# Kernel tuning notes

Hardware: AMD Instinct MI355X
Metric: run time of the kernel (lower is better)

The kernel has to match this reference:

```python
import jax, jax.numpy as jnp
import numpy as np

ROUTING = 3
N_VERTEX = 32
D_CAP = 16
MULT_D = 64
B = 64
T_DIMS = {"text": 128, "audio": 512, "video": 256, "frames": 256}


def _xavier(key, shape):
    # torch xavier_normal_ on (T, n, MULT_d, d_c): receptive = MULT_d*d_c
    T, n, j, d = shape
    recep = j * d
    std = np.sqrt(2.0 / (n * recep + T * recep))
    return jax.random.normal(key, shape, dtype=jnp.float32) * std


def setup_inputs() -> dict:
    key = jax.random.key(0)
    ks = jax.random.split(key, 8)
    inp = {}
    for i, (name, T) in enumerate(T_DIMS.items()):
        inp[name] = jax.random.normal(ks[i], (B, T, MULT_D), dtype=jnp.float32)
    wnames = ["W_tpc", "W_apc", "W_vpc", "W_fpc"]
    for i, (name, (_, T)) in enumerate(zip(wnames, T_DIMS.items())):
        inp[name] = _xavier(ks[4 + i], (T, N_VERTEX, MULT_D, D_CAP))
    return inp


def _route(pri, routing):
    # pri: [B, T, n, d_c]; routing uses detached (stop-gradient) capsules
    pri_sg = jax.lax.stop_gradient(pri)
    Bn, T, n, d = pri.shape
    b = jnp.zeros((Bn, T, n), dtype=pri.dtype)
    for _ in range(routing):
        rc = jax.nn.softmax(b, axis=2)                      # [B, T, n]
        v = jnp.tanh(jnp.einsum('btnd,btn->bnd', pri_sg, rc))
        b = b + jnp.einsum('bnd,btnd->btn', v, pri_sg)      # agreement update
    rc = jnp.softmax(b, axis=2) if False else jax.nn.softmax(b, axis=2)
    # final vertex uses non-detached capsules with last routing coefficients
    return jnp.tanh(jnp.einsum('btnd,btn->bnd', pri, rc))


def reference(text, audio, video, frames, W_tpc, W_apc, W_vpc, W_fpc):
    outs = []
    for x, W in ((text, W_tpc), (audio, W_apc), (video, W_vpc), (frames, W_fpc)):
        pri = jnp.einsum('btj,tnjd->btnd', x, W)  # primary capsules [B,T,n,d_c]
        outs.append(_route(pri, ROUTING))
    return tuple(outs)
```

## Files before the change

kernel.cpp:

```cpp
#include <hip/hip_runtime.h>


typedef __attribute__((ext_vector_type(8))) short short8;
typedef __attribute__((ext_vector_type(4))) float floatx4;

#define PRI_BYTES 75497472ull

static __device__ __forceinline__ unsigned short f2bf(float f) {
  union { float f; unsigned int i; } v;
  v.f = f;
  unsigned int x = v.i;
  return (unsigned short)((x + 0x7fffu + ((x >> 16) & 1u)) >> 16);
}

__global__ __launch_bounds__(256) void pri_kernel(
    const float* __restrict__ x0, const float* __restrict__ x1,
    const float* __restrict__ x2, const float* __restrict__ x3,
    const float* __restrict__ w0, const float* __restrict__ w1,
    const float* __restrict__ w2, const float* __restrict__ w3,
    unsigned short* __restrict__ priAll) {
  __shared__ unsigned short wb[256 * 72];
  __shared__ unsigned short sc[4][16][136];

  int blk = blockIdx.x;
  int tid = threadIdx.x;

  int tpair = blk >> 1, half = blk & 1;
  const float* x;
  const float* W;
  unsigned short* priT;
  int T, t;
  if (tpair < 128)      { x = x0; W = w0; priT = priAll;               T = 128; t = tpair; }
  else if (tpair < 640) { x = x1; W = w1; priT = priAll + 4194304ull;  T = 512; t = tpair - 128; }
  else if (tpair < 896) { x = x2; W = w2; priT = priAll + 20971520ull; T = 256; t = tpair - 640; }
  else                  { x = x3; W = w3; priT = priAll + 29360128ull; T = 256; t = tpair - 896; }
  priT += (size_t)t * 32768;

  {
    const floatx4* Wf4 = (const floatx4*)(W + (size_t)t * 32768);
    unsigned int* wb32 = (unsigned int*)wb;
#pragma unroll
    for (int it = 0; it < 8; ++it) {
      int idx = it * 256 + tid;
      int nl = idx >> 7, jp = (idx >> 2) & 31, dq = idx & 3;
      int ng = half * 16 + nl;
      floatx4 fa = Wf4[ng * 256 + (2 * jp) * 4 + dq];
      floatx4 fb = Wf4[ng * 256 + (2 * jp + 1) * 4 + dq];
      int rbase = nl * 16 + dq * 4;
#pragma unroll
      for (int k = 0; k < 4; ++k) {
        unsigned int dw = (unsigned int)f2bf(fa[k]) | ((unsigned int)f2bf(fb[k]) << 16);
        wb32[(rbase + k) * 36 + jp] = dw;
      }
    }
  }

  int lane = tid & 63, mt = tid >> 6;
  int m = lane & 15, q = lane >> 4;
  short8 afrag[2];
  {
    const float* xrow = x + ((size_t)(mt * 16 + m) * T + t) * 64;
#pragma unroll
    for (int s = 0; s < 2; ++s) {
      const floatx4* xp = (const floatx4*)(xrow + s * 32 + q * 8);
      floatx4 u0 = xp[0], u1 = xp[1];
      afrag[s][0] = (short)f2bf(u0[0]); afrag[s][1] = (short)f2bf(u0[1]);
      afrag[s][2] = (short)f2bf(u0[2]); afrag[s][3] = (short)f2bf(u0[3]);
      afrag[s][4] = (short)f2bf(u1[0]); afrag[s][5] = (short)f2bf(u1[1]);
      afrag[s][6] = (short)f2bf(u1[2]); afrag[s][7] = (short)f2bf(u1[3]);
    }
  }
  __syncthreads();

  for (int g = 0; g < 2; ++g) {
#pragma unroll
    for (int k = 0; k < 8; ++k) {
      int nt = g * 8 + k;
      const short8* b0p = (const short8*)&wb[(nt * 16 + m) * 72 + q * 8];
      const short8* b1p = (const short8*)&wb[(nt * 16 + m) * 72 + 32 + q * 8];
      short8 bf0 = *b0p, bf1 = *b1p;
      floatx4 acc = {0.f, 0.f, 0.f, 0.f};
      acc = __builtin_amdgcn_mfma_f32_16x16x32_bf16(afrag[0], bf0, acc, 0, 0, 0);
      acc = __builtin_amdgcn_mfma_f32_16x16x32_bf16(afrag[1], bf1, acc, 0, 0, 0);
#pragma unroll
      for (int reg = 0; reg < 4; ++reg)
        sc[mt][q * 4 + reg][k * 16 + m] = f2bf(acc[reg]);
    }
#pragma unroll
    for (int i = 0; i < 4; ++i) {
      int bl = (lane >> 4) + i * 4;
      int sh = (lane & 15) * 8;
      short8 v = *(const short8*)&sc[mt][bl][sh];
      *(short8*)(priT + (size_t)(mt * 16 + bl) * 512 + half * 256 + g * 128 + sh) = v;
    }
  }
}

__global__ __launch_bounds__(1024) void route_kernel(
    const unsigned short* __restrict__ priAll, float* __restrict__ out) {
  __shared__ float Sl[32][640];
  __shared__ float Vc_s[544];

  int blk = blockIdx.x;
  int mod = blk & 3, b = blk >> 2;
  size_t poff; int T;
  if (mod == 0)      { poff = 0ull;         T = 128; }
  else if (mod == 1) { poff = 4194304ull;   T = 512; }
  else if (mod == 2) { poff = 20971520ull;  T = 256; }
  else               { poff = 29360128ull;  T = 256; }

  const unsigned short* priM = priAll + poff + (size_t)b * 512;

  int tid = threadIdx.x;
  int n = tid & 31, g = tid >> 5;
  int nbase = n * 17;

  if (tid < 544) Vc_s[tid] = 0.f;
  __syncthreads();

  for (int pass = 0; pass < 4; ++pass) {
    float Vc[16];
#pragma unroll
    for (int d = 0; d < 16; ++d) Vc[d] = Vc_s[nbase + d];

    float acc[16];
#pragma unroll
    for (int d = 0; d < 16; ++d) acc[d] = 0.f;

    const unsigned short* pr = priM + (size_t)(g * 2) * 32768 + n * 16;
    uint4 c0a = ((const uint4*)pr)[0], c0b = ((const uint4*)pr)[1];
    uint4 c1a = ((const uint4*)(pr + 32768))[0], c1b = ((const uint4*)(pr + 32768))[1];

    for (int t0 = g * 2; t0 < T; t0 += 64) {
      uint4 n0a, n0b, n1a, n1b;
      if (t0 + 64 < T) {
        const unsigned short* pn = priM + (size_t)(t0 + 64) * 32768 + n * 16;
        n0a = ((const uint4*)pn)[0]; n0b = ((const uint4*)pn)[1];
        n1a = ((const uint4*)(pn + 32768))[0]; n1b = ((const uint4*)(pn + 32768))[1];
      }

#pragma unroll
      for (int tt = 0; tt < 2; ++tt) {
        uint4 ca = tt ? c1a : c0a;
        uint4 cb = tt ? c1b : c0b;
        float p[16];
        {
          unsigned int wds[8] = {ca.x, ca.y, ca.z, ca.w, cb.x, cb.y, cb.z, cb.w};
#pragma unroll
          for (int k = 0; k < 8; ++k) {
            union { unsigned int u; float f; } lo, hi;
            lo.u = wds[k] << 16;
            hi.u = wds[k] & 0xffff0000u;
            p[2 * k] = lo.f;
            p[2 * k + 1] = hi.f;
          }
        }
        float logit = 0.f;
#pragma unroll
        for (int d = 0; d < 16; ++d) logit += p[d] * Vc[d];
        float mx = logit;
#pragma unroll
        for (int o = 16; o >= 1; o >>= 1) mx = fmaxf(mx, __shfl_xor(mx, o, 32));
        float e = __expf(logit - mx);
        float s = e;
#pragma unroll
        for (int o = 16; o >= 1; o >>= 1) s += __shfl_xor(s, o, 32);
        float rc = e / s;
#pragma unroll
        for (int d = 0; d < 16; ++d) acc[d] += rc * p[d];
      }

      if (t0 + 64 < T) { c0a = n0a; c0b = n0b; c1a = n1a; c1b = n1b; }
    }

#pragma unroll
    for (int d = 0; d < 16; ++d) Sl[g][nbase + d] = acc[d];
    __syncthreads();

    if (tid < 512) {
      int nn = tid >> 4, dd = tid & 15;
      int idx = nn * 17 + dd;
      float s = 0.f;
#pragma unroll
      for (int gg = 0; gg < 32; ++gg) s += Sl[gg][idx];
      float v = tanhf(s);
      if (pass == 3) out[(size_t)(mod * 64 + b) * 512 + tid] = v;
      else Vc_s[idx] += v;
    }
    __syncthreads();
  }
}

extern "C" void kernel_launch(void* const* d_in, const int* in_sizes, int n_in,
                              void* d_out, int out_size, void* d_ws, size_t ws_size,
                              hipStream_t stream) {
  const float* x0 = (const float*)d_in[0];
  const float* x1 = (const float*)d_in[1];
  const float* x2 = (const float*)d_in[2];
  const float* x3 = (const float*)d_in[3];
  const float* w0 = (const float*)d_in[4];
  const float* w1 = (const float*)d_in[5];
  const float* w2 = (const float*)d_in[6];
  const float* w3 = (const float*)d_in[7];

  unsigned short* pri = (unsigned short*)d_ws;

  pri_kernel<<<2304, 256, 0, stream>>>(x0, x1, x2, x3, w0, w1, w2, w3, pri);
  route_kernel<<<256, 1024, 0, stream>>>(pri, (float*)d_out);
}
```

Baseline: 262.8 us.

## Process two timesteps per pri block with prefetched weights; simplify routing softmax

Each pri_kernel block now handles two consecutive timesteps, so the grid is halved. The second timestep's weights are loaded into registers while the first is computed, hiding global load latency behind the MFMA work. The route kernel walks one timestep per 32-thread group with a stride of 32 timesteps and drops the max-subtraction in the softmax, removing five shuffles per timestep. Without the max-subtraction the exponentials could overflow if the logits grow large. The extra register arrays per thread may also reduce occupancy.

```diff
diff --git a/kernel.cpp b/kernel.cpp
--- a/kernel.cpp
+++ b/kernel.cpp
@@ -3,8 +3,6 @@
 
 typedef __attribute__((ext_vector_type(8))) short short8;
 typedef __attribute__((ext_vector_type(4))) float floatx4;
-
-#define PRI_BYTES 75497472ull
 
 static __device__ __forceinline__ unsigned short f2bf(float f) {
   union { float f; unsigned int i; } v;
@@ -25,75 +23,130 @@
   int blk = blockIdx.x;
   int tid = threadIdx.x;
 
-  int tpair = blk >> 1, half = blk & 1;
+  int pair = blk >> 1, half = blk & 1;
   const float* x;
   const float* W;
   unsigned short* priT;
-  int T, t;
-  if (tpair < 128)      { x = x0; W = w0; priT = priAll;               T = 128; t = tpair; }
-  else if (tpair < 640) { x = x1; W = w1; priT = priAll + 4194304ull;  T = 512; t = tpair - 128; }
-  else if (tpair < 896) { x = x2; W = w2; priT = priAll + 20971520ull; T = 256; t = tpair - 640; }
-  else                  { x = x3; W = w3; priT = priAll + 29360128ull; T = 256; t = tpair - 896; }
-  priT += (size_t)t * 32768;
-
+  int T, t0;
+  if (pair < 64)       { x = x0; W = w0; priT = priAll;               T = 128; t0 = 2 * pair; }
+  else if (pair < 320) { x = x1; W = w1; priT = priAll + 4194304ull;  T = 512; t0 = 2 * (pair - 64); }
+  else if (pair < 448) { x = x2; W = w2; priT = priAll + 20971520ull; T = 256; t0 = 2 * (pair - 320); }
+  else                 { x = x3; W = w3; priT = priAll + 29360128ull; T = 256; t0 = 2 * (pair - 448); }
+  unsigned short* priT0 = priT + (size_t)t0 * 32768;
+  unsigned short* priT1 = priT + (size_t)(t0 + 1) * 32768;
+
+  int lane = tid & 63, mt = tid >> 6;
+  int m = lane & 15, q = lane >> 4;
+
+  floatx4 xv[8];
   {
-    const floatx4* Wf4 = (const floatx4*)(W + (size_t)t * 32768);
-    unsigned int* wb32 = (unsigned int*)wb;
+    const float* xrow = x + ((size_t)(mt * 16 + m) * T + t0) * 64;
+#pragma unroll
+    for (int tt = 0; tt < 2; ++tt)
+#pragma unroll
+      for (int s = 0; s < 2; ++s) {
+        const floatx4* xp = (const floatx4*)(xrow + tt * 64 + s * 32 + q * 8);
+        xv[tt * 4 + s * 2]     = xp[0];
+        xv[tt * 4 + s * 2 + 1] = xp[1];
+      }
+  }
+
+  floatx4 wra[8], wrb[8];
+  {
+    const floatx4* Wf = (const floatx4*)(W + (size_t)t0 * 32768);
 #pragma unroll
     for (int it = 0; it < 8; ++it) {
       int idx = it * 256 + tid;
       int nl = idx >> 7, jp = (idx >> 2) & 31, dq = idx & 3;
       int ng = half * 16 + nl;
-      floatx4 fa = Wf4[ng * 256 + (2 * jp) * 4 + dq];
-      floatx4 fb = Wf4[ng * 256 + (2 * jp + 1) * 4 + dq];
-      int rbase = nl * 16 + dq * 4;
-#pragma unroll
-      for (int k = 0; k < 4; ++k) {
-        unsigned int dw = (unsigned int)f2bf(fa[k]) | ((unsigned int)f2bf(fb[k]) << 16);
-        wb32[(rbase + k) * 36 + jp] = dw;
-      }
-    }
-  }
-
-  int lane = tid & 63, mt = tid >> 6;
-  int m = lane & 15, q = lane >> 4;
-  short8 afrag[2];
+      wra[it] = Wf[ng * 256 + (2 * jp) * 4 + dq];
+      wrb[it] = Wf[ng * 256 + (2 * jp + 1) * 4 + dq];
+    }
+  }
+
+  short8 afrag[2][2];
+#pragma unroll
+  for (int tt = 0; tt < 2; ++tt)
+#pragma unroll
+    for (int s = 0; s < 2; ++s) {
+      floatx4 u0 = xv[tt * 4 + s * 2], u1 = xv[tt * 4 + s * 2 + 1];
+      short8 a;
+      a[0] = (short)f2bf(u0[0]); a[1] = (short)f2bf(u0[1]);
+      a[2] = (short)f2bf(u0[2]); a[3] = (short)f2bf(u0[3]);
+      a[4] = (short)f2bf(u1[0]); a[5] = (short)f2bf(u1[1]);
+      a[6] = (short)f2bf(u1[2]); a[7] = (short)f2bf(u1[3]);
+      afrag[tt][s] = a;
+    }
+
+  unsigned int* wb32 = (unsigned int*)wb;
+
+#pragma unroll
+  for (int it = 0; it < 8; ++it) {
+    int idx = it * 256 + tid;
+    int nl = idx >> 7, jp = (idx >> 2) & 31, dq = idx & 3;
+    int rbase = nl * 16 + dq * 4;
+#pragma unroll
+    for (int k = 0; k < 4; ++k) {
+      unsigned int dw = (unsigned int)f2bf(wra[it][k]) | ((unsigned int)f2bf(wrb[it][k]) << 16);
+      wb32[(rbase + k) * 36 + jp] = dw;
+    }
+  }
+  __syncthreads();
+
   {
-    const float* xrow = x + ((size_t)(mt * 16 + m) * T + t) * 64;
-#pragma unroll
-    for (int s = 0; s < 2; ++s) {
-      const floatx4* xp = (const floatx4*)(xrow + s * 32 + q * 8);
-      floatx4 u0 = xp[0], u1 = xp[1];
-      afrag[s][0] = (short)f2bf(u0[0]); afrag[s][1] = (short)f2bf(u0[1]);
-      afrag[s][2] = (short)f2bf(u0[2]); afrag[s][3] = (short)f2bf(u0[3]);
-      afrag[s][4] = (short)f2bf(u1[0]); afrag[s][5] = (short)f2bf(u1[1]);
-      afrag[s][6] = (short)f2bf(u1[2]); afrag[s][7] = (short)f2bf(u1[3]);
-    }
-  }
-  __syncthreads();
-
-  for (int g = 0; g < 2; ++g) {
-#pragma unroll
-    for (int k = 0; k < 8; ++k) {
-      int nt = g * 8 + k;
-      const short8* b0p = (const short8*)&wb[(nt * 16 + m) * 72 + q * 8];
-      const short8* b1p = (const short8*)&wb[(nt * 16 + m) * 72 + 32 + q * 8];
-      short8 bf0 = *b0p, bf1 = *b1p;
-      floatx4 acc = {0.f, 0.f, 0.f, 0.f};
-      acc = __builtin_amdgcn_mfma_f32_16x16x32_bf16(afrag[0], bf0, acc, 0, 0, 0);
-      acc = __builtin_amdgcn_mfma_f32_16x16x32_bf16(afrag[1], bf1, acc, 0, 0, 0);
-#pragma unroll
-      for (int reg = 0; reg < 4; ++reg)
-        sc[mt][q * 4 + reg][k * 16 + m] = f2bf(acc[reg]);
-    }
-#pragma unroll
-    for (int i = 0; i < 4; ++i) {
-      int bl = (lane >> 4) + i * 4;
-      int sh = (lane & 15) * 8;
-      short8 v = *(const short8*)&sc[mt][bl][sh];
-      *(short8*)(priT + (size_t)(mt * 16 + bl) * 512 + half * 256 + g * 128 + sh) = v;
-    }
-  }
+    const floatx4* Wf = (const floatx4*)(W + (size_t)(t0 + 1) * 32768);
+#pragma unroll
+    for (int it = 0; it < 8; ++it) {
+      int idx = it * 256 + tid;
+      int nl = idx >> 7, jp = (idx >> 2) & 31, dq = idx & 3;
+      int ng = half * 16 + nl;
+      wra[it] = Wf[ng * 256 + (2 * jp) * 4 + dq];
+      wrb[it] = Wf[ng * 256 + (2 * jp + 1) * 4 + dq];
+    }
+  }
+
+  auto compute_t = [&](const short8& a0, const short8& a1, unsigned short* dst) {
+    for (int g2 = 0; g2 < 2; ++g2) {
+#pragma unroll
+      for (int k = 0; k < 8; ++k) {
+        int nt = g2 * 8 + k;
+        const short8* b0p = (const short8*)&wb[(nt * 16 + m) * 72 + q * 8];
+        const short8* b1p = (const short8*)&wb[(nt * 16 + m) * 72 + 32 + q * 8];
+        short8 bf0 = *b0p, bf1 = *b1p;
+        floatx4 acc = {0.f, 0.f, 0.f, 0.f};
+        acc = __builtin_amdgcn_mfma_f32_16x16x32_bf16(a0, bf0, acc, 0, 0, 0);
+        acc = __builtin_amdgcn_mfma_f32_16x16x32_bf16(a1, bf1, acc, 0, 0, 0);
+#pragma unroll
+        for (int reg = 0; reg < 4; ++reg)
+          sc[mt][q * 4 + reg][k * 16 + m] = f2bf(acc[reg]);
+      }
+#pragma unroll
+      for (int i = 0; i < 4; ++i) {
+        int bl = (lane >> 4) + i * 4;
+        int sh = (lane & 15) * 8;
+        short8 v = *(const short8*)&sc[mt][bl][sh];
+        *(short8*)(dst + (size_t)(mt * 16 + bl) * 512 + half * 256 + g2 * 128 + sh) = v;
+      }
+    }
+  };
+
+  compute_t(afrag[0][0], afrag[0][1], priT0);
+  __syncthreads();
+
+#pragma unroll
+  for (int it = 0; it < 8; ++it) {
+    int idx = it * 256 + tid;
+    int nl = idx >> 7, jp = (idx >> 2) & 31, dq = idx & 3;
+    int rbase = nl * 16 + dq * 4;
+#pragma unroll
+    for (int k = 0; k < 4; ++k) {
+      unsigned int dw = (unsigned int)f2bf(wra[it][k]) | ((unsigned int)f2bf(wrb[it][k]) << 16);
+      wb32[(rbase + k) * 36 + jp] = dw;
+    }
+  }
+  __syncthreads();
+
+  compute_t(afrag[1][0], afrag[1][1], priT1);
 }
 
 __global__ __launch_bounds__(1024) void route_kernel(
@@ -118,6 +171,8 @@
   if (tid < 544) Vc_s[tid] = 0.f;
   __syncthreads();
 
+  int iters = T >> 5;
+
   for (int pass = 0; pass < 4; ++pass) {
     float Vc[16];
 #pragma unroll
@@ -127,50 +182,38 @@
 #pragma unroll
     for (int d = 0; d < 16; ++d) acc[d] = 0.f;
 
-    const unsigned short* pr = priM + (size_t)(g * 2) * 32768 + n * 16;
-    uint4 c0a = ((const uint4*)pr)[0], c0b = ((const uint4*)pr)[1];
-    uint4 c1a = ((const uint4*)(pr + 32768))[0], c1b = ((const uint4*)(pr + 32768))[1];
-
-    for (int t0 = g * 2; t0 < T; t0 += 64) {
-      uint4 n0a, n0b, n1a, n1b;
-      if (t0 + 64 < T) {
-        const unsigned short* pn = priM + (size_t)(t0 + 64) * 32768 + n * 16;
-        n0a = ((const uint4*)pn)[0]; n0b = ((const uint4*)pn)[1];
-        n1a = ((const uint4*)(pn + 32768))[0]; n1b = ((const uint4*)(pn + 32768))[1];
-      }
-
-#pragma unroll
-      for (int tt = 0; tt < 2; ++tt) {
-        uint4 ca = tt ? c1a : c0a;
-        uint4 cb = tt ? c1b : c0b;
-        float p[16];
-        {
-          unsigned int wds[8] = {ca.x, ca.y, ca.z, ca.w, cb.x, cb.y, cb.z, cb.w};
-#pragma unroll
-          for (int k = 0; k < 8; ++k) {
-            union { unsigned int u; float f; } lo, hi;
-            lo.u = wds[k] << 16;
-            hi.u = wds[k] & 0xffff0000u;
-            p[2 * k] = lo.f;
-            p[2 * k + 1] = hi.f;
-          }
+    const uint4* pr = (const uint4*)(priM + (size_t)g * 32768 + n * 16);
+    uint4 ca = pr[0], cb = pr[1];
+
+    for (int it = 0; it < iters; ++it) {
+      uint4 na, nb;
+      bool more = (it + 1 < iters);
+      if (more) { na = pr[131072]; nb = pr[131073]; }
+
+      float p[16];
+      {
+        unsigned int wds[8] = {ca.x, ca.y, ca.z, ca.w, cb.x, cb.y, cb.z, cb.w};
+#pragma unroll
+        for (int k = 0; k < 8; ++k) {
+          union { unsigned int u; float f; } lo, hi;
+          lo.u = wds[k] << 16;
+          hi.u = wds[k] & 0xffff0000u;
+          p[2 * k] = lo.f;
+          p[2 * k + 1] = hi.f;
         }
-        float logit = 0.f;
-#pragma unroll
-        for (int d = 0; d < 16; ++d) logit += p[d] * Vc[d];
-        float mx = logit;
-#pragma unroll
-        for (int o = 16; o >= 1; o >>= 1) mx = fmaxf(mx, __shfl_xor(mx, o, 32));
-        float e = __expf(logit - mx);
-        float s = e;
-#pragma unroll
-        for (int o = 16; o >= 1; o >>= 1) s += __shfl_xor(s, o, 32);
-        float rc = e / s;
-#pragma unroll
-        for (int d = 0; d < 16; ++d) acc[d] += rc * p[d];
-      }
-
-      if (t0 + 64 < T) { c0a = n0a; c0b = n0b; c1a = n1a; c1b = n1b; }
+      }
+      float logit = 0.f;
+#pragma unroll
+      for (int d = 0; d < 16; ++d) logit += p[d] * Vc[d];
+      float e = __expf(logit);
+      float s = e;
+#pragma unroll
+      for (int o = 16; o >= 1; o >>= 1) s += __shfl_xor(s, o, 32);
+      float rc = e / s;
+#pragma unroll
+      for (int d = 0; d < 16; ++d) acc[d] += rc * p[d];
+
+      if (more) { ca = na; cb = nb; pr += 131072; }
     }
 
 #pragma unroll
@@ -205,6 +248,6 @@
 
   unsigned short* pri = (unsigned short*)d_ws;
 
-  pri_kernel<<<2304, 256, 0, stream>>>(x0, x1, x2, x3, w0, w1, w2, w3, pri);
+  pri_kernel<<<1152, 256, 0, stream>>>(x0, x1, x2, x3, w0, w1, w2, w3, pri);
   route_kernel<<<256, 1024, 0, stream>>>(pri, (float*)d_out);
 }
```

Measured after the change: 249.3 us. -5.2%, faster.
